# Optimization experiments

Hardware: AMD Instinct MI355X
Metric: run time of the kernel (lower is better)

## Reference

```python
import jax, jax.numpy as jnp
import numpy as np

B, L, D, V, NL = 32, 40, 128, 32000, 2


def setup_inputs() -> dict:
    key = jax.random.key(0)
    ks = jax.random.split(key, 7)
    return {
        "q": jax.random.randint(ks[0], (B, L), 0, V),
        "a": jax.random.randint(ks[1], (B, L), 0, V),
        "embed": jax.random.normal(ks[2], (V, D), dtype=jnp.float32),
        "conv_w": jax.random.normal(ks[3], (NL, 4, 1, 1, 4, 3), dtype=jnp.float32) * 0.3,
        "conv_b": jax.random.normal(ks[4], (NL, 4), dtype=jnp.float32) * 0.1,
        "lin_w": jax.random.normal(ks[5], (2, 2 * D * D), dtype=jnp.float32) * 0.01,
        "lin_b": jax.random.normal(ks[6], (2,), dtype=jnp.float32) * 0.01,
    }


def _density(xe):
    # xe: (B, L, D) -> (B, L, D, D); outer product normalized by squared norm
    outer = jnp.einsum('bli,blj->blij', xe, xe)
    dot = jnp.sum(xe * xe, axis=-1)[..., None, None]  # (B, L, 1, 1)
    return outer / (dot + 1e-4)


def _gate_conv(inp, w, b):
    # inp: (B, 1, 2D, D); w: (1, 1, 4, 3); stride (2,1), pad (1,1) -> (B, 1, D, D)
    y = jax.lax.conv_general_dilated(
        inp, w, window_strides=(2, 1), padding=((1, 1), (1, 1)),
        dimension_numbers=('NCHW', 'OIHW', 'NCHW'))
    return y + b[None, :, None, None]


def _cnn_lstm(x, conv_w, conv_b):
    # x: (B, L, D, D); conv_w: (NL, 4, 1, 1, 4, 3); conv_b: (NL, 4)
    b, l, d, _ = x.shape
    pre = x
    for li in range(conv_w.shape[0]):
        ws, bs = conv_w[li], conv_b[li]

        def step(carry, xt):
            h, c = carry
            inp = jnp.concatenate([xt, h], axis=2)  # (B, 1, 2D, D)
            fg = jax.nn.sigmoid(_gate_conv(inp, ws[0], bs[0:1]))
            ig = jax.nn.sigmoid(_gate_conv(inp, ws[1], bs[1:2]))
            og = jax.nn.sigmoid(_gate_conv(inp, ws[2], bs[2:3]))
            cs = jnp.tanh(_gate_conv(inp, ws[3], bs[3:4]))
            c = fg * c + ig * cs
            h = og * jnp.tanh(c)
            return (h, c), h

        h0 = jnp.zeros((b, 1, d, d), pre.dtype)
        xs = jnp.swapaxes(pre, 0, 1)[:, :, None]  # (L, B, 1, D, D)
        _, hs = jax.lax.scan(step, (h0, h0), xs)
        pre = jnp.swapaxes(hs[:, :, 0], 0, 1)  # (B, L, D, D)
    return pre


def reference(q, a, embed, conv_w, conv_b, lin_w, lin_b):
    bs = q.shape[0]
    q_d = _density(embed[q])  # (B, L, D, D)
    a_d = _density(embed[a])
    q_o = _cnn_lstm(q_d, conv_w, conv_b).reshape(bs, L, -1)  # (B, L, D*D)
    a_o = _cnn_lstm(a_d, conv_w, conv_b).reshape(bs, L, -1)
    q_p = jnp.max(q_o, axis=1)  # max pool over sequence
    a_p = jnp.max(a_o, axis=1)
    qa = jnp.concatenate([q_p, a_p], axis=1)  # (B, 2*D*D)
    score = qa @ lin_w.T + lin_b
    return jax.nn.log_softmax(score, axis=1)
```

## Files before the change

kernel.cpp:

```cpp
#include <hip/hip_runtime.h>
#include <math.h>

#define BB 32
#define LL 40
#define DD 128
#define NSB 64
#define NU  (NSB * LL)
#define PLANE (DD * DD)
#define SLAB ((size_t)NSB * PLANE)

typedef unsigned short u16;
typedef unsigned int u32;

__device__ __forceinline__ u16 f2bf(float f) {
    union { float f; unsigned u; } v; v.f = f;
    unsigned u = v.u;
    u += 0x7fff + ((u >> 16) & 1);
    return (u16)(u >> 16);
}
__device__ __forceinline__ float bf2f(u16 b) {
    union { unsigned u; float f; } v; v.u = ((unsigned)b) << 16;
    return v.f;
}
__device__ __forceinline__ float rcpf(float x) { return __builtin_amdgcn_rcpf(x); }
__device__ __forceinline__ float sigm(float x)  { return rcpf(1.f + __expf(-x)); }
__device__ __forceinline__ float tanhs(float x) { return fmaf(2.f, rcpf(1.f + __expf(-2.f * x)), -1.f); }

__global__ void prep_kernel(const int* __restrict__ q, const int* __restrict__ a,
                            const float* __restrict__ embed,
                            float* __restrict__ xe_all, float* __restrict__ inv_all) {
    int u = blockIdx.x * 4 + (threadIdx.x >> 6);
    int lane = threadIdx.x & 63;
    if (u >= NU) return;
    int sb = u / LL, t = u % LL;
    int s = sb >> 5, b = sb & 31;
    const int* idx = s ? a : q;
    int e = idx[b * LL + t];
    const float* row = embed + (size_t)e * DD;
    float v0 = row[lane], v1 = row[lane + 64];
    xe_all[(size_t)u * DD + lane] = v0;
    xe_all[(size_t)u * DD + lane + 64] = v1;
    float d = v0 * v0 + v1 * v1;
    #pragma unroll
    for (int o = 32; o; o >>= 1) d += __shfl_down(d, o);
    if (lane == 0) inv_all[u] = 1.f / (d + 1e-4f);
}

__global__ __launch_bounds__(512)
void sep0_kernel(const float* __restrict__ xe_all, const float* __restrict__ inv_all,
                 const float* __restrict__ conv_w, const float* __restrict__ conv_b,
                 u16* __restrict__ h1) {
    const int nchunk = (63 * NSB) / 8;
    const int logical = ((int)blockIdx.x % 8) * nchunk + (int)blockIdx.x / 8;
    const int i  = logical % 63;
    const int sb = logical / 63;
    const int tid = threadIdx.x;
    const int cp = tid & 63;
    const int t0 = tid >> 6;
    const int c0 = 2 * cp;

    __shared__ float xe_s[LL][DD];
    __shared__ float U[LL][12];
    __shared__ u32 gfo_l[LL][DD];
    __shared__ u32 gic_l[LL][DD / 2];
    __shared__ float wls[48];

    if (tid < 48) wls[tid] = conv_w[tid];
    float b4[4];
    #pragma unroll
    for (int k = 0; k < 4; ++k) b4[k] = conv_b[k];

    const float2* xsrc = (const float2*)(xe_all + (size_t)(sb * LL) * DD);
    for (int e = tid; e < LL * DD / 2; e += 512)
        ((float2*)xe_s)[e] = xsrc[e];
    __syncthreads();

    if (tid < LL * 12) {
        int t = tid / 12, k = tid - t * 12;
        int g = k / 3, kw = k - g * 3;
        int base = 2 * i - 1;
        float s = 0.f;
        #pragma unroll
        for (int kh = 0; kh < 4; ++kh) {
            int r = base + kh;
            if (r >= 0) s = fmaf(wls[g * 12 + kh * 3 + kw], xe_s[t][r], s);
        }
        U[t][k] = s * inv_all[sb * LL + t];
    }
    __syncthreads();

    #pragma unroll
    for (int k5 = 0; k5 < 5; ++k5) {
        const int t = t0 + 8 * k5;
        float4 u0 = *(const float4*)&U[t][0];
        float4 u1 = *(const float4*)&U[t][4];
        float4 u2 = *(const float4*)&U[t][8];
        float xl = cp > 0 ? xe_s[t][c0 - 1] : 0.f;
        float xm = xe_s[t][c0];
        float xr = xe_s[t][c0 + 1];
        float x2 = cp < 63 ? xe_s[t][c0 + 2] : 0.f;
        float a0 = fmaf(u0.x, xl, fmaf(u0.y, xm, fmaf(u0.z, xr, b4[0])));
        float a1 = fmaf(u0.w, xl, fmaf(u1.x, xm, fmaf(u1.y, xr, b4[1])));
        float a2 = fmaf(u1.z, xl, fmaf(u1.w, xm, fmaf(u2.x, xr, b4[2])));
        float a3 = fmaf(u2.y, xl, fmaf(u2.z, xm, fmaf(u2.w, xr, b4[3])));
        float d0 = fmaf(u0.x, xm, fmaf(u0.y, xr, fmaf(u0.z, x2, b4[0])));
        float d1 = fmaf(u0.w, xm, fmaf(u1.x, xr, fmaf(u1.y, x2, b4[1])));
        float d2 = fmaf(u1.z, xm, fmaf(u1.w, xr, fmaf(u2.x, x2, b4[2])));
        float d3 = fmaf(u2.y, xm, fmaf(u2.z, xr, fmaf(u2.w, x2, b4[3])));
        float fg0 = sigm(a0), ic0 = sigm(a1) * tanhs(a3), og0 = sigm(a2);
        float fg1 = sigm(d0), ic1 = sigm(d1) * tanhs(d3), og1 = sigm(d2);
        u32 f0 = (u32)f2bf(fg0) | ((u32)f2bf(og0) << 16);
        u32 f1 = (u32)f2bf(fg1) | ((u32)f2bf(og1) << 16);
        *(uint2*)&gfo_l[t][c0] = make_uint2(f0, f1);
        gic_l[t][cp] = (u32)f2bf(ic0) | ((u32)f2bf(ic1) << 16);
    }
    __syncthreads();

    if (tid < DD) {
        const int c = tid;
        u16* hp = h1 + SLAB + (size_t)sb * PLANE + (size_t)i * DD + c;
        float cc = 0.f;
        #pragma unroll 4
        for (int t = 0; t < LL; ++t) {
            u32 v = gfo_l[t][c];
            u32 icp = gic_l[t][c >> 1];
            float fg = bf2f((u16)v), og = bf2f((u16)(v >> 16));
            float ic = bf2f((u16)(icp >> ((c & 1) * 16)));
            cc = fg * cc + ic;
            *hp = f2bf(og * tanhs(cc));
            hp += SLAB;
        }
    }
}

__global__ __launch_bounds__(512, 8)
void fused_level_kernel(const float* __restrict__ xe_all, const float* __restrict__ inv_all,
                        const u16* __restrict__ xt_h1,
                        u16* __restrict__ h_own,
                        float* __restrict__ pool,
                        const float* __restrict__ conv_w, const float* __restrict__ conv_b,
                        int layer, int r0, int nr) {
    const int nchunk = (nr * NSB) / 8;
    const int logical = ((int)blockIdx.x % 8) * nchunk + (int)blockIdx.x / 8;
    const int i  = r0 + logical % nr;
    const int sb = logical / nr;
    const int tid = threadIdx.x;
    const int cp = tid & 63;
    const int t0 = tid >> 6;
    const int c0 = 2 * cp;

    __shared__ u32 gfo_l[LL][DD];
    __shared__ u32 gic_l[LL][DD / 2];

    float w[48], b4[4];
    #pragma unroll
    for (int k = 0; k < 48; ++k) w[k] = conv_w[layer * 48 + k];
    #pragma unroll
    for (int k = 0; k < 4; ++k) b4[k] = conv_b[layer * 4 + k];

    const u16* sp[4];
    bool dens[4];
    int wrow[4];
    #pragma unroll
    for (int kh = 0; kh < 4; ++kh) {
        const int wr = 2 * i - 1 + kh;
        wrow[kh] = wr;
        dens[kh] = false;
        sp[kh] = nullptr;
        if (wr >= 0 && wr < 2 * DD) {
            if (wr < DD) {
                if (layer == 0) dens[kh] = true;
                else sp[kh] = xt_h1 + (size_t)(t0 + 1) * SLAB + (size_t)sb * PLANE + (size_t)wr * DD;
            } else {
                sp[kh] = h_own + (size_t)t0 * SLAB + (size_t)sb * PLANE + (size_t)(wr - DD) * DD;
            }
        }
    }
    const bool cL = (cp > 0), cR = (cp < 63);
    const bool anyd = (layer == 0) && (2 * i - 1 < DD);
    const float* xe_u = xe_all + ((size_t)sb * LL + t0) * DD;
    const float* ip   = inv_all + sb * LL + t0;

    for (int k = 0; k < 5; ++k) {
        const int t = t0 + 8 * k;
        float a0 = b4[0], a1 = b4[1], a2 = b4[2], a3 = b4[3];
        float d0 = b4[0], d1 = b4[1], d2 = b4[2], d3 = b4[3];
        float x_1 = 0.f, xA = 0.f, xB = 0.f, x2 = 0.f, invv = 0.f;
        if (anyd) {
            invv = *ip;
            x_1 = cL ? xe_u[c0 - 1] : 0.f;
            xA = xe_u[c0]; xB = xe_u[c0 + 1];
            x2 = cR ? xe_u[c0 + 2] : 0.f;
        }
        #pragma unroll
        for (int kh = 0; kh < 4; ++kh) {
            float vA, vB0, vB1, vC;
            if (dens[kh]) {
                float p = invv * xe_u[wrow[kh]];
                vA = p * x_1; vB0 = p * xA; vB1 = p * xB; vC = p * x2;
            } else if (sp[kh]) {
                u32 pb = *(const u32*)(sp[kh] + c0);
                u32 up = __shfl_up(pb, 1);
                u32 dn = __shfl_down(pb, 1);
                vB0 = bf2f((u16)pb); vB1 = bf2f((u16)(pb >> 16));
                vA = cL ? bf2f((u16)(up >> 16)) : 0.f;
                vC = cR ? bf2f((u16)dn) : 0.f;
            } else {
                vA = 0.f; vB0 = 0.f; vB1 = 0.f; vC = 0.f;
            }
            a0 = fmaf(vA,  w[kh*3+0], a0);    a0 = fmaf(vB0, w[kh*3+1], a0);    a0 = fmaf(vB1, w[kh*3+2], a0);
            a1 = fmaf(vA,  w[12+kh*3+0], a1); a1 = fmaf(vB0, w[12+kh*3+1], a1); a1 = fmaf(vB1, w[12+kh*3+2], a1);
            a2 = fmaf(vA,  w[24+kh*3+0], a2); a2 = fmaf(vB0, w[24+kh*3+1], a2); a2 = fmaf(vB1, w[24+kh*3+2], a2);
            a3 = fmaf(vA,  w[36+kh*3+0], a3); a3 = fmaf(vB0, w[36+kh*3+1], a3); a3 = fmaf(vB1, w[36+kh*3+2], a3);
            d0 = fmaf(vB0, w[kh*3+0], d0);    d0 = fmaf(vB1, w[kh*3+1], d0);    d0 = fmaf(vC, w[kh*3+2], d0);
            d1 = fmaf(vB0, w[12+kh*3+0], d1); d1 = fmaf(vB1, w[12+kh*3+1], d1); d1 = fmaf(vC, w[12+kh*3+2], d1);
            d2 = fmaf(vB0, w[24+kh*3+0], d2); d2 = fmaf(vB1, w[24+kh*3+1], d2); d2 = fmaf(vC, w[24+kh*3+2], d2);
            d3 = fmaf(vB0, w[36+kh*3+0], d3); d3 = fmaf(vB1, w[36+kh*3+1], d3); d3 = fmaf(vC, w[36+kh*3+2], d3);
        }
        float fg0 = sigm(a0), ic0 = sigm(a1) * tanhs(a3), og0 = sigm(a2);
        float fg1 = sigm(d0), ic1 = sigm(d1) * tanhs(d3), og1 = sigm(d2);
        u32 f0 = (u32)f2bf(fg0) | ((u32)f2bf(og0) << 16);
        u32 f1 = (u32)f2bf(fg1) | ((u32)f2bf(og1) << 16);
        *(uint2*)&gfo_l[t][c0] = make_uint2(f0, f1);
        gic_l[t][cp] = (u32)f2bf(ic0) | ((u32)f2bf(ic1) << 16);
        #pragma unroll
        for (int kh = 0; kh < 4; ++kh) if (sp[kh]) sp[kh] += 8 * SLAB;
        if (anyd) { xe_u += 8 * DD; ip += 8; }
    }
    __syncthreads();

    if (tid < DD) {
        const int c = tid;
        u16* hp = h_own + SLAB + (size_t)sb * PLANE + (size_t)i * DD + c;
        float cc = 0.f, pr = -1e30f;
        #pragma unroll 4
        for (int t = 0; t < LL; ++t) {
            u32 v = gfo_l[t][c];
            u32 icp = gic_l[t][c >> 1];
            float fg = bf2f((u16)v), og = bf2f((u16)(v >> 16));
            float ic = bf2f((u16)(icp >> ((c & 1) * 16)));
            cc = fg * cc + ic;
            float hn = og * tanhs(cc);
            *hp = f2bf(hn);
            pr = fmaxf(pr, hn);
            hp += SLAB;
        }
        if (pool) pool[(size_t)sb * PLANE + (size_t)i * DD + c] = pr;
    }
}

__device__ __forceinline__
float tail_px(const float (*wp)[130], const float* wls, const float* bls,
              int lr, int c, float& creg, float& pr) {
    float a0 = bls[0], a1 = bls[1], a2 = bls[2], a3 = bls[3];
    #pragma unroll
    for (int kh = 0; kh < 4; ++kh) {
        #pragma unroll
        for (int kw = 0; kw < 3; ++kw) {
            float v = wp[lr + kh][c + kw];
            a0 = fmaf(v, wls[kh*3+kw], a0);
            a1 = fmaf(v, wls[12+kh*3+kw], a1);
            a2 = fmaf(v, wls[24+kh*3+kw], a2);
            a3 = fmaf(v, wls[36+kh*3+kw], a3);
        }
    }
    float fg = sigm(a0), ig = sigm(a1), og = sigm(a2), cs = tanhs(a3);
    creg = fg * creg + ig * cs;
    float hn = og * tanhs(creg);
    pr = fmaxf(pr, hn);
    return hn;
}

__global__ __launch_bounds__(640)
void tail5_kernel(const u16* __restrict__ hsrc, u16* __restrict__ hdst,
                  float* __restrict__ pool,
                  const float* __restrict__ conv_w, const float* __restrict__ conv_b,
                  int layer) {
    const int sb = blockIdx.x;
    const int tid = threadIdx.x;
    const int slot = tid >> 7;
    const int c = tid & 127;
    const int r = 123 + slot;
    __shared__ float win[2][12][130];
    __shared__ float wls[48], bls[4];
    if (tid < 48) wls[tid] = conv_w[layer * 48 + tid];
    if (tid < 4)  bls[tid] = conv_b[layer * 4 + tid];
    for (int e = tid; e < 2 * 12 * 130; e += 640) ((float*)win)[e] = 0.f;

    const bool ldr = tid < 384;
    const int lrow = tid >> 6;
    const int lcp = tid & 63;
    const u16* gsrc = hsrc + (size_t)sb * PLANE + (size_t)(117 + lrow) * DD + 2 * lcp;
    u32 pre = 0;
    if (ldr) pre = *(const u32*)gsrc;

    const int lr0 = 2 * slot;
    u16* hd = hdst ? hdst + SLAB + (size_t)sb * PLANE + (size_t)r * DD + c : nullptr;
    float creg = 0.f, pr = -1e30f;

    for (int t = 0; t < LL; ++t) {
        const int p = t & 1;
        __syncthreads();
        if (ldr) {
            win[p][lrow][2 * lcp + 1] = bf2f((u16)pre);
            win[p][lrow][2 * lcp + 2] = bf2f((u16)(pre >> 16));
        }
        __syncthreads();
        if (ldr && t + 1 < LL)
            pre = *(const u32*)(gsrc + (size_t)(t + 1) * SLAB);
        float hn = tail_px(win[p], wls, bls, lr0, c, creg, pr);
        win[p ^ 1][6 + slot][c + 1] = hn;
        if (hd) { *hd = f2bf(hn); hd += SLAB; }
    }
    if (pool) pool[(size_t)sb * PLANE + (size_t)r * DD + c] = pr;
}

__global__ void final_kernel(const float* __restrict__ pool,
                             const float* __restrict__ lin_w,
                             const float* __restrict__ lin_b,
                             float* __restrict__ out) {
    const int b = blockIdx.x;
    const int tid = threadIdx.x;
    const int DD2 = DD * DD;
    const float* pq = pool + (size_t)b * DD2;
    const float* pa = pool + (size_t)(BB + b) * DD2;
    float s0 = 0.f, s1 = 0.f;
    for (int j = tid; j < DD2; j += 256) {
        float vq = pq[j], va = pa[j];
        s0 += vq * lin_w[j]           + va * lin_w[DD2 + j];
        s1 += vq * lin_w[2 * DD2 + j] + va * lin_w[3 * DD2 + j];
    }
    #pragma unroll
    for (int o = 32; o; o >>= 1) {
        s0 += __shfl_down(s0, o);
        s1 += __shfl_down(s1, o);
    }
    __shared__ float sh0[4], sh1[4];
    int wid = tid >> 6, lane = tid & 63;
    if (lane == 0) { sh0[wid] = s0; sh1[wid] = s1; }
    __syncthreads();
    if (tid == 0) {
        float a0 = sh0[0] + sh0[1] + sh0[2] + sh0[3] + lin_b[0];
        float a1 = sh1[0] + sh1[1] + sh1[2] + sh1[3] + lin_b[1];
        float m = fmaxf(a0, a1);
        float lse = m + logf(expf(a0 - m) + expf(a1 - m));
        out[b * 2 + 0] = a0 - lse;
        out[b * 2 + 1] = a1 - lse;
    }
}

extern "C" void kernel_launch(void* const* d_in, const int* in_sizes, int n_in,
                              void* d_out, int out_size, void* d_ws, size_t ws_size,
                              hipStream_t stream) {
    const int*   q      = (const int*)d_in[0];
    const int*   a      = (const int*)d_in[1];
    const float* embed  = (const float*)d_in[2];
    const float* conv_w = (const float*)d_in[3];
    const float* conv_b = (const float*)d_in[4];
    const float* lin_w  = (const float*)d_in[5];
    const float* lin_b  = (const float*)d_in[6];
    float* out = (float*)d_out;

    float* ws      = (float*)d_ws;
    float* pool    = ws;
    float* xe_all  = pool + (size_t)NSB * PLANE;
    float* inv_all = xe_all + (size_t)NU * DD;
    u16*   h1      = (u16*)(inv_all + NU);
    u16*   h2      = h1 + (size_t)(LL + 1) * SLAB;

    hipMemsetAsync(h1, 0, SLAB * sizeof(u16), stream);
    hipMemsetAsync(h2, 0, SLAB * sizeof(u16), stream);

    prep_kernel<<<(NU + 3) / 4, 256, 0, stream>>>(q, a, embed, xe_all, inv_all);

    const int levr[5][2] = {{0,63},{63,32},{95,16},{111,8},{119,4}};

    for (int layer = 0; layer < 2; ++layer) {
        const u16* xt = layer ? h1 : nullptr;
        u16* hh       = layer ? h2 : h1;
        float* pl     = layer ? pool : nullptr;
        for (int k = 0; k < 5; ++k) {
            const int r0 = levr[k][0], nr = levr[k][1];
            if (layer == 0 && k == 0) {
                sep0_kernel<<<63 * NSB, 512, 0, stream>>>(
                    xe_all, inv_all, conv_w, conv_b, h1);
            } else {
                fused_level_kernel<<<nr * NSB, 512, 0, stream>>>(
                    xe_all, inv_all, xt, hh, pl, conv_w, conv_b, layer, r0, nr);
            }
        }
        tail5_kernel<<<NSB, 640, 0, stream>>>(hh, layer ? nullptr : h1,
                                              pl, conv_w, conv_b, layer);
    }

    final_kernel<<<BB, 256, 0, stream>>>(pool, lin_w, lin_b, out);
}
```

Measured before the change: 464.9 us.

## Switch hidden-state storage to fp16 and compute gate convolutions with packed half2 math

```diff
diff --git a/kernel.cpp b/kernel.cpp
--- a/kernel.cpp
+++ b/kernel.cpp
@@ -1,4 +1,5 @@
 #include <hip/hip_runtime.h>
+#include <hip/hip_fp16.h>
 #include <math.h>
 
 #define BB 32
@@ -12,16 +13,20 @@
 typedef unsigned short u16;
 typedef unsigned int u32;
 
-__device__ __forceinline__ u16 f2bf(float f) {
-    union { float f; unsigned u; } v; v.f = f;
-    unsigned u = v.u;
-    u += 0x7fff + ((u >> 16) & 1);
-    return (u16)(u >> 16);
-}
-__device__ __forceinline__ float bf2f(u16 b) {
-    union { unsigned u; float f; } v; v.u = ((unsigned)b) << 16;
-    return v.f;
-}
+__device__ __forceinline__ u16 f2h(float f) {
+    __half h = __float2half(f);
+    union { __half h; u16 u; } v; v.h = h; return v.u;
+}
+__device__ __forceinline__ float h2f(u16 b) {
+    union { u16 u; __half h; } v; v.u = b; return __half2float(v.h);
+}
+__device__ __forceinline__ u32 h2bits(__half2 h) {
+    union { __half2 h; u32 u; } v; v.h = h; return v.u;
+}
+__device__ __forceinline__ __half2 bits2h(u32 b) {
+    union { u32 u; __half2 h; } v; v.u = b; return v.h;
+}
+
 __device__ __forceinline__ float rcpf(float x) { return __builtin_amdgcn_rcpf(x); }
 __device__ __forceinline__ float sigm(float x)  { return rcpf(1.f + __expf(-x)); }
 __device__ __forceinline__ float tanhs(float x) { return fmaf(2.f, rcpf(1.f + __expf(-2.f * x)), -1.f); }
@@ -88,6 +93,14 @@
         U[t][k] = s * inv_all[sb * LL + t];
     }
     __syncthreads();
+
+    auto f2bf = [](float f) -> u16 {
+        union { float f; unsigned u; } v; v.f = f;
+        unsigned u = v.u; u += 0x7fff + ((u >> 16) & 1); return (u16)(u >> 16);
+    };
+    auto bf2f = [](u16 b) -> float {
+        union { unsigned u; float f; } v; v.u = ((unsigned)b) << 16; return v.f;
+    };
 
     #pragma unroll
     for (int k5 = 0; k5 < 5; ++k5) {
@@ -126,14 +139,14 @@
             u32 icp = gic_l[t][c >> 1];
             float fg = bf2f((u16)v), og = bf2f((u16)(v >> 16));
             float ic = bf2f((u16)(icp >> ((c & 1) * 16)));
-            cc = fg * cc + ic;
-            *hp = f2bf(og * tanhs(cc));
+            cc = fmaf(fg, cc, ic);
+            *hp = f2h(og * tanhs(cc));
             hp += SLAB;
         }
     }
 }
 
-__global__ __launch_bounds__(512, 8)
+__global__ __launch_bounds__(512, 4)
 void fused_level_kernel(const float* __restrict__ xe_all, const float* __restrict__ inv_all,
                         const u16* __restrict__ xt_h1,
                         u16* __restrict__ h_own,
@@ -149,14 +162,19 @@
     const int t0 = tid >> 6;
     const int c0 = 2 * cp;
 
-    __shared__ u32 gfo_l[LL][DD];
-    __shared__ u32 gic_l[LL][DD / 2];
-
-    float w[48], b4[4];
-    #pragma unroll
-    for (int k = 0; k < 48; ++k) w[k] = conv_w[layer * 48 + k];
-    #pragma unroll
-    for (int k = 0; k < 4; ++k) b4[k] = conv_b[layer * 4 + k];
+    __shared__ u32 gf_l[LL][DD / 2];
+    __shared__ u32 go_l[LL][DD / 2];
+    __shared__ u32 gi_l[LL][DD / 2];
+
+    __half2 wb[48];
+    #pragma unroll
+    for (int k = 0; k < 48; ++k) wb[k] = __float2half2_rn(conv_w[layer * 48 + k]);
+    __half2 bb[4];
+    #pragma unroll
+    for (int k = 0; k < 4; ++k) bb[k] = __float2half2_rn(conv_b[layer * 4 + k]);
+    const __half2 one2 = __float2half2_rn(1.f);
+    const __half2 two2 = __float2half2_rn(2.f);
+    const __half2 none2 = __float2half2_rn(-1.f);
 
     const u16* sp[4];
     bool dens[4];
@@ -177,14 +195,15 @@
         }
     }
     const bool cL = (cp > 0), cR = (cp < 63);
+    const u32 maskA = cL ? 0xFFFFFFFFu : 0xFFFF0000u;
+    const u32 maskC = cR ? 0xFFFFFFFFu : 0x0000FFFFu;
     const bool anyd = (layer == 0) && (2 * i - 1 < DD);
     const float* xe_u = xe_all + ((size_t)sb * LL + t0) * DD;
     const float* ip   = inv_all + sb * LL + t0;
 
     for (int k = 0; k < 5; ++k) {
         const int t = t0 + 8 * k;
-        float a0 = b4[0], a1 = b4[1], a2 = b4[2], a3 = b4[3];
-        float d0 = b4[0], d1 = b4[1], d2 = b4[2], d3 = b4[3];
+        __half2 acc0 = bb[0], acc1 = bb[1], acc2 = bb[2], acc3 = bb[3];
         float x_1 = 0.f, xA = 0.f, xB = 0.f, x2 = 0.f, invv = 0.f;
         if (anyd) {
             invv = *ip;
@@ -194,35 +213,49 @@
         }
         #pragma unroll
         for (int kh = 0; kh < 4; ++kh) {
-            float vA, vB0, vB1, vC;
+            u32 pA, pB, pC;
+            bool have = true;
             if (dens[kh]) {
                 float p = invv * xe_u[wrow[kh]];
-                vA = p * x_1; vB0 = p * xA; vB1 = p * xB; vC = p * x2;
+                pA = h2bits(__floats2half2_rn(p * x_1, p * xA));
+                pB = h2bits(__floats2half2_rn(p * xA, p * xB));
+                pC = h2bits(__floats2half2_rn(p * xB, p * x2));
             } else if (sp[kh]) {
                 u32 pb = *(const u32*)(sp[kh] + c0);
                 u32 up = __shfl_up(pb, 1);
                 u32 dn = __shfl_down(pb, 1);
-                vB0 = bf2f((u16)pb); vB1 = bf2f((u16)(pb >> 16));
-                vA = cL ? bf2f((u16)(up >> 16)) : 0.f;
-                vC = cR ? bf2f((u16)dn) : 0.f;
+                pA = __builtin_amdgcn_alignbit(pb, up, 16) & maskA;
+                pB = pb;
+                pC = __builtin_amdgcn_alignbit(dn, pb, 16) & maskC;
             } else {
-                vA = 0.f; vB0 = 0.f; vB1 = 0.f; vC = 0.f;
+                have = false; pA = pB = pC = 0;
             }
-            a0 = fmaf(vA,  w[kh*3+0], a0);    a0 = fmaf(vB0, w[kh*3+1], a0);    a0 = fmaf(vB1, w[kh*3+2], a0);
-            a1 = fmaf(vA,  w[12+kh*3+0], a1); a1 = fmaf(vB0, w[12+kh*3+1], a1); a1 = fmaf(vB1, w[12+kh*3+2], a1);
-            a2 = fmaf(vA,  w[24+kh*3+0], a2); a2 = fmaf(vB0, w[24+kh*3+1], a2); a2 = fmaf(vB1, w[24+kh*3+2], a2);
-            a3 = fmaf(vA,  w[36+kh*3+0], a3); a3 = fmaf(vB0, w[36+kh*3+1], a3); a3 = fmaf(vB1, w[36+kh*3+2], a3);
-            d0 = fmaf(vB0, w[kh*3+0], d0);    d0 = fmaf(vB1, w[kh*3+1], d0);    d0 = fmaf(vC, w[kh*3+2], d0);
-            d1 = fmaf(vB0, w[12+kh*3+0], d1); d1 = fmaf(vB1, w[12+kh*3+1], d1); d1 = fmaf(vC, w[12+kh*3+2], d1);
-            d2 = fmaf(vB0, w[24+kh*3+0], d2); d2 = fmaf(vB1, w[24+kh*3+1], d2); d2 = fmaf(vC, w[24+kh*3+2], d2);
-            d3 = fmaf(vB0, w[36+kh*3+0], d3); d3 = fmaf(vB1, w[36+kh*3+1], d3); d3 = fmaf(vC, w[36+kh*3+2], d3);
-        }
-        float fg0 = sigm(a0), ic0 = sigm(a1) * tanhs(a3), og0 = sigm(a2);
-        float fg1 = sigm(d0), ic1 = sigm(d1) * tanhs(d3), og1 = sigm(d2);
-        u32 f0 = (u32)f2bf(fg0) | ((u32)f2bf(og0) << 16);
-        u32 f1 = (u32)f2bf(fg1) | ((u32)f2bf(og1) << 16);
-        *(uint2*)&gfo_l[t][c0] = make_uint2(f0, f1);
-        gic_l[t][cp] = (u32)f2bf(ic0) | ((u32)f2bf(ic1) << 16);
+            if (have) {
+                __half2 hA = bits2h(pA), hB = bits2h(pB), hC = bits2h(pC);
+                acc0 = __hfma2(hA, wb[kh*3+0], acc0);
+                acc0 = __hfma2(hB, wb[kh*3+1], acc0);
+                acc0 = __hfma2(hC, wb[kh*3+2], acc0);
+                acc1 = __hfma2(hA, wb[12+kh*3+0], acc1);
+                acc1 = __hfma2(hB, wb[12+kh*3+1], acc1);
+                acc1 = __hfma2(hC, wb[12+kh*3+2], acc1);
+                acc2 = __hfma2(hA, wb[24+kh*3+0], acc2);
+                acc2 = __hfma2(hB, wb[24+kh*3+1], acc2);
+                acc2 = __hfma2(hC, wb[24+kh*3+2], acc2);
+                acc3 = __hfma2(hA, wb[36+kh*3+0], acc3);
+                acc3 = __hfma2(hB, wb[36+kh*3+1], acc3);
+                acc3 = __hfma2(hC, wb[36+kh*3+2], acc3);
+            }
+        }
+        __half2 e;
+        e = h2exp(__hneg2(acc0)); __half2 fg2 = h2rcp(__hadd2(one2, e));
+        e = h2exp(__hneg2(acc1)); __half2 ig2 = h2rcp(__hadd2(one2, e));
+        e = h2exp(__hneg2(acc2)); __half2 og2 = h2rcp(__hadd2(one2, e));
+        e = h2exp(__hneg2(__hadd2(acc3, acc3)));
+        __half2 cs2 = __hfma2(two2, h2rcp(__hadd2(one2, e)), none2);
+        __half2 ic2 = __hmul2(ig2, cs2);
+        gf_l[t][cp] = h2bits(fg2);
+        go_l[t][cp] = h2bits(og2);
+        gi_l[t][cp] = h2bits(ic2);
         #pragma unroll
         for (int kh = 0; kh < 4; ++kh) if (sp[kh]) sp[kh] += 8 * SLAB;
         if (anyd) { xe_u += 8 * DD; ip += 8; }
@@ -231,17 +264,17 @@
 
     if (tid < DD) {
         const int c = tid;
+        const int sh = (c & 1) * 16;
         u16* hp = h_own + SLAB + (size_t)sb * PLANE + (size_t)i * DD + c;
         float cc = 0.f, pr = -1e30f;
         #pragma unroll 4
         for (int t = 0; t < LL; ++t) {
-            u32 v = gfo_l[t][c];
-            u32 icp = gic_l[t][c >> 1];
-            float fg = bf2f((u16)v), og = bf2f((u16)(v >> 16));
-            float ic = bf2f((u16)(icp >> ((c & 1) * 16)));
-            cc = fg * cc + ic;
+            float fg = h2f((u16)(gf_l[t][c >> 1] >> sh));
+            float og = h2f((u16)(go_l[t][c >> 1] >> sh));
+            float ic = h2f((u16)(gi_l[t][c >> 1] >> sh));
+            cc = fmaf(fg, cc, ic);
             float hn = og * tanhs(cc);
-            *hp = f2bf(hn);
+            *hp = f2h(hn);
             pr = fmaxf(pr, hn);
             hp += SLAB;
         }
@@ -302,15 +335,15 @@
         const int p = t & 1;
         __syncthreads();
         if (ldr) {
-            win[p][lrow][2 * lcp + 1] = bf2f((u16)pre);
-            win[p][lrow][2 * lcp + 2] = bf2f((u16)(pre >> 16));
+            win[p][lrow][2 * lcp + 1] = h2f((u16)pre);
+            win[p][lrow][2 * lcp + 2] = h2f((u16)(pre >> 16));
         }
         __syncthreads();
         if (ldr && t + 1 < LL)
             pre = *(const u32*)(gsrc + (size_t)(t + 1) * SLAB);
         float hn = tail_px(win[p], wls, bls, lr0, c, creg, pr);
         win[p ^ 1][6 + slot][c + 1] = hn;
-        if (hd) { *hd = f2bf(hn); hd += SLAB; }
+        if (hd) { *hd = f2h(hn); hd += SLAB; }
     }
     if (pool) pool[(size_t)sb * PLANE + (size_t)r * DD + c] = pr;
 }
```

Measured after the change: 503.2 us. +8.3%, slower.
